# Kernel tuning notes

Measured on AMD Instinct MI355X. Metric: run time of the kernel, lower is better.

The kernel has to match this reference:

```python
import jax, jax.numpy as jnp
import numpy as np
import math

ITER = 5
ALPHA = 2.0
C = 128
B, H, W = 64, 40, 96


def _conv(x, w, pad_h, pad_w):
    # x: [B,C,H,W], w: [O,I,kh,kw]
    return jax.lax.conv_general_dilated(
        x, w, window_strides=(1, 1),
        padding=[(pad_h, pad_h), (pad_w, pad_w)],
        dimension_numbers=("NCHW", "OIHW", "NCHW"))


def setup_inputs() -> dict:
    key = jax.random.key(0)
    k = jax.random.split(key, 5)
    bound = math.sqrt(2.0 / (C * 9 * 5))
    x = jax.random.normal(k[0], (B, C, H, W), dtype=jnp.float32)
    wd = jax.random.uniform(k[1], (ITER, C, C, 1, 9), jnp.float32, -bound, bound)
    wu = jax.random.uniform(k[2], (ITER, C, C, 1, 9), jnp.float32, -bound, bound)
    wr = jax.random.uniform(k[3], (ITER, C, C, 9, 1), jnp.float32, -bound, bound)
    wl = jax.random.uniform(k[4], (ITER, C, C, 9, 1), jnp.float32, -bound, bound)
    return {"x": x, "wd": wd, "wu": wu, "wr": wr, "wl": wl}


def reference(x, wd, wu, wr, wl):
    h, w = x.shape[-2], x.shape[-1]
    y = x
    # downward: circular shift of rows by +offset == roll(-offset) along H
    for i in range(ITER):
        off = h // 2 ** (ITER - i)
        y = y + ALPHA * jax.nn.relu(_conv(jnp.roll(y, -off, axis=2), wd[i], 0, 4))
    # upward: rows shifted by -offset == roll(+offset)
    for i in range(ITER):
        off = h // 2 ** (ITER - i)
        y = y + ALPHA * jax.nn.relu(_conv(jnp.roll(y, off, axis=2), wu[i], 0, 4))
    # rightward: cols shifted by +offset == roll(-offset) along W
    for i in range(ITER):
        off = w // 2 ** (ITER - i)
        y = y + ALPHA * jax.nn.relu(_conv(jnp.roll(y, -off, axis=3), wr[i], 4, 0))
    # leftward: cols shifted by -offset == roll(+offset)
    for i in range(ITER):
        off = w // 2 ** (ITER - i)
        y = y + ALPHA * jax.nn.relu(_conv(jnp.roll(y, off, axis=3), wl[i], 4, 0))
    return y
```

## Files before the change

### kernel.cpp

```cpp
#include <hip/hip_runtime.h>
#include <cstdint>
#include <cstddef>

#define CH 128
#define HH 40
#define WW 96
#define BB 64
#define HW (HH*WW)
#define CHW ((size_t)CH*HW)

typedef _Float16 half8  __attribute__((ext_vector_type(8)));
typedef _Float16 half4v __attribute__((ext_vector_type(4)));
typedef float    float4v __attribute__((ext_vector_type(4)));

#define MFMA16(a,b,c) __builtin_amdgcn_mfma_f32_16x16x32_f16((a),(b),(c),0,0,0)

#define SPLIT_SCALE 2048.0f
#define INV_SPLIT   (1.0f/2048.0f)

#define NHWC_HALVES (BB*HH*WW*CH)
#define WSTEP_F     (CH*CH*9)
#define WFRAG_HALVES (20*9*4*8*64*8)

__device__ __forceinline__ void gload16(const _Float16* g, _Float16* l) {
    __builtin_amdgcn_global_load_lds(
        (const __attribute__((address_space(1))) void*)g,
        (__attribute__((address_space(3))) void*)l,
        16, 0, 0);
}


__global__ __launch_bounds__(256) void prep_weights(
    const float* __restrict__ wd, const float* __restrict__ wu,
    const float* __restrict__ wr, const float* __restrict__ wl,
    _Float16* __restrict__ WH, _Float16* __restrict__ WM)
{
    const int bx = blockIdx.x;
    const int s = bx / 9, t = bx % 9;
    const float* src;
    if (s < 5)       src = wd + (size_t)s*WSTEP_F;
    else if (s < 10) src = wu + (size_t)(s-5)*WSTEP_F;
    else if (s < 15) src = wr + (size_t)(s-10)*WSTEP_F;
    else             src = wl + (size_t)(s-15)*WSTEP_F;

    for (int idx = threadIdx.x; idx < 2048; idx += 256) {
        const int lane = idx & 63;
        const int mt   = (idx >> 6) & 7;
        const int kq   = idx >> 9;
        const int co   = mt*16 + (lane & 15);
        const int cib  = kq*32 + (lane >> 4)*8;
        const int F    = ((((s*9 + t)*4 + kq)*8 + mt)*64 + lane)*8;
        #pragma unroll
        for (int j = 0; j < 8; ++j) {
            const float w = src[(size_t)(co*CH + (cib + j))*9 + t];
            const _Float16 h = (_Float16)w;
            WH[F + j] = h;
            WM[F + j] = (_Float16)((w - (float)h) * SPLIT_SCALE);
        }
    }
}

__global__ __launch_bounds__(256) void prep_acts(
    const float* __restrict__ x, _Float16* __restrict__ H, _Float16* __restrict__ M)
{
    __shared__ float tile[CH][33];
    const int wt = blockIdx.x, h = blockIdx.y, b = blockIdx.z;
    const int tid = threadIdx.x;
    {
        const int wl = tid & 31, c0 = tid >> 5;
        for (int it = 0; it < 16; ++it) {
            const int ci = it*8 + c0;
            tile[ci][wl] = x[((size_t)(b*CH + ci)*HH + h)*WW + wt*32 + wl];
        }
    }
    __syncthreads();
    {
        const int ci = tid & 127, w0 = tid >> 7;
        for (int it = 0; it < 16; ++it) {
            const int wl = it*2 + w0;
            const float v = tile[ci][wl];
            const _Float16 hh = (_Float16)v;
            const int o = ((b*HH + h)*WW + wt*32 + wl)*CH + ci;
            H[o] = hh;
            M[o] = (_Float16)((v - (float)hh) * SPLIT_SCALE);
        }
    }
}

__global__ __launch_bounds__(256, 2) void hconv_mfma(
    const _Float16* __restrict__ srcH, const _Float16* __restrict__ srcM,
    _Float16* __restrict__ dstH, _Float16* __restrict__ dstM,
    const _Float16* __restrict__ WH, const _Float16* __restrict__ WM,
    int s, int hoff)
{
    __shared__ _Float16 sB[2][104*128];
    const int h = blockIdx.x, b = blockIdx.y;
    const int tid = threadIdx.x;
    const int hp = (h + hoff) % HH;
    const int lane = tid & 63, wave = tid >> 6;

    {
        const int rr = lane >> 4, slot = lane & 15;
        #pragma unroll
        for (int k = 0; k < 6; ++k) {
            const int c = wave*6 + k;
            const int rbase = 4 + 4*c;
            const int row = rbase + rr;
            const size_t goff = ((size_t)(b*HH + hp)*WW + (rbase - 4))*CH;
            const int so = rr*CH + ((slot ^ (row & 7))*8);
            gload16(srcH + goff + so, (_Float16*)&sB[0][rbase*128]);
            gload16(srcM + goff + so, (_Float16*)&sB[1][rbase*128]);
        }
        const int zrow = (wave & 1)*100;
        const int arr  = wave >> 1;
        *(half8*)&sB[arr][zrow*128 + lane*8] = (half8){};
    }
    __syncthreads();

    const int n = lane & 15, quad = lane >> 4;
    const int mgrp = wave & 1, ngrp = wave >> 1;
    const int qs = quad*8;
#define BADDR(row, kq) ((row)*128 + ((((kq)*32) + qs) ^ ((((row) & 7)) << 3)))

    float4v acc0[4][3], acc1[4][3];
    #pragma unroll
    for (int i = 0; i < 4; ++i)
        #pragma unroll
        for (int j = 0; j < 3; ++j) {
            acc0[i][j] = (float4v){0.f,0.f,0.f,0.f};
            acc1[i][j] = (float4v){0.f,0.f,0.f,0.f};
        }

    int rowb[3];
    #pragma unroll
    for (int j = 0; j < 3; ++j) rowb[j] = (ngrp*3 + j)*16 + n;

    const size_t Fb = (size_t)s*147456 + (size_t)(mgrp*2048 + lane*8);

    half8 Wh[2][4], Wm[2][4];
    #pragma unroll
    for (int i = 0; i < 4; ++i) {
        Wh[0][i] = *(const half8*)(WH + Fb + i*512);
        Wm[0][i] = *(const half8*)(WM + Fb + i*512);
    }
    half8 pbh = *(const half8*)&sB[0][BADDR(rowb[0], 0)];
    half8 pbm = *(const half8*)&sB[1][BADDR(rowb[0], 0)];

    for (int t = 0; t < 9; ++t) {
        #pragma unroll
        for (int kq = 0; kq < 4; ++kq) {
            const int it  = t*4 + kq;
            const int itn = (it < 35) ? it + 1 : 35;
            const int pc  = kq & 1;
            const int pn  = pc ^ 1;
            {
                const _Float16* nH = WH + Fb + (size_t)itn*4096;
                const _Float16* nM = WM + Fb + (size_t)itn*4096;
                #pragma unroll
                for (int i = 0; i < 4; ++i) {
                    Wh[pn][i] = *(const half8*)(nH + i*512);
                    Wm[pn][i] = *(const half8*)(nM + i*512);
                }
            }
            const int tn = itn >> 2, kqn = itn & 3;
            #pragma unroll
            for (int j = 0; j < 3; ++j) {
                const half8 bh = pbh, bm = pbm;
                int nro;
                if (j < 2) nro = BADDR(rowb[j+1] + t, kq);
                else       nro = BADDR(rowb[0] + tn, kqn);
                pbh = *(const half8*)&sB[0][nro];
                pbm = *(const half8*)&sB[1][nro];
                __builtin_amdgcn_s_setprio(1);
                #pragma unroll
                for (int i = 0; i < 4; ++i) {
                    acc0[i][j] = MFMA16(Wh[pc][i], bh, acc0[i][j]);
                    acc1[i][j] = MFMA16(Wh[pc][i], bm, acc1[i][j]);
                    acc1[i][j] = MFMA16(Wm[pc][i], bh, acc1[i][j]);
                }
                __builtin_amdgcn_s_setprio(0);
            }
        }
    }
#undef BADDR

    const int spbase = (b*HH + h)*WW;
    #pragma unroll
    for (int i = 0; i < 4; ++i) {
        const int co = (mgrp*4 + i)*16 + quad*4;
        #pragma unroll
        for (int j = 0; j < 3; ++j) {
            const int w  = (ngrp*3 + j)*16 + n;
            const int sp = (spbase + w)*CH + co;
            const half4v oh = *(const half4v*)(srcH + sp);
            const half4v om = *(const half4v*)(srcM + sp);
            half4v zh, zm;
            #pragma unroll
            for (int r = 0; r < 4; ++r) {
                const float v = acc0[i][j][r] + acc1[i][j][r]*INV_SPLIT;
                const float y = (float)oh[r] + (float)om[r]*INV_SPLIT;
                const float z = y + 2.0f*fmaxf(v, 0.0f);
                const _Float16 a = (_Float16)z;
                zh[r] = a;
                zm[r] = (_Float16)((z - (float)a)*SPLIT_SCALE);
            }
            *(half4v*)(dstH + sp) = zh;
            *(half4v*)(dstM + sp) = zm;
        }
    }
}

__global__ __launch_bounds__(256, 2) void vconv_mfma(
    const _Float16* __restrict__ srcH, const _Float16* __restrict__ srcM,
    _Float16* __restrict__ dstH, _Float16* __restrict__ dstM,
    const _Float16* __restrict__ WH, const _Float16* __restrict__ WM,
    int s, int woff, int final, float* __restrict__ f32out)
{
    __shared__ _Float16 sB[2][96*128];
    const int wp = blockIdx.x, b = blockIdx.y;
    const int tid = threadIdx.x;
    const int lane = tid & 63, wave = tid >> 6;

    {
        const int rr = lane >> 4, slot = lane & 15;
        for (int k = wave; k < 20; k += 4) {
            const int col = (k >= 10);
            const int c = k - col*10;
            const int rbase = col*48 + 4 + 4*c;
            const int h0 = 4*c;
            const int wsrc = (wp*2 + col + woff) % WW;
            const size_t goff = ((size_t)(b*HH + h0)*WW + wsrc)*CH;
            const int row = rbase + rr;
            const int so = rr*(WW*CH) + ((slot ^ (row & 7))*8);
            gload16(srcH + goff + so, (_Float16*)&sB[0][rbase*128]);
            gload16(srcM + goff + so, (_Float16*)&sB[1][rbase*128]);
        }
        const int zrow = (wave & 1)*44 + (wave >> 1)*48;
        *(half8*)&sB[0][zrow*128 + lane*8] = (half8){};
        *(half8*)&sB[1][zrow*128 + lane*8] = (half8){};
    }
    __syncthreads();

    const int n = lane & 15, quad = lane >> 4;
    const int mgrp = wave & 1;
    const int jbase = (wave >> 1)*3;
    const bool has3 = (wave >> 1) == 0;
    const int qs = quad*8;
#define BADDR(row, kq) ((row)*128 + ((((kq)*32) + qs) ^ ((((row) & 7)) << 3)))

    float4v acc0[4][3], acc1[4][3];
    #pragma unroll
    for (int i = 0; i < 4; ++i)
        #pragma unroll
        for (int j = 0; j < 3; ++j) {
            acc0[i][j] = (float4v){0.f,0.f,0.f,0.f};
            acc1[i][j] = (float4v){0.f,0.f,0.f,0.f};
        }

    int rowbse[3];
    #pragma unroll
    for (int jj = 0; jj < 3; ++jj) {
        int o = (jbase + jj)*16 + n;
        if (o > 79) o = 79;
        const int col = (o >= 40);
        rowbse[jj] = o + 8*col;
    }

    const size_t Fb = (size_t)s*147456 + (size_t)(mgrp*2048 + lane*8);

    half8 Wh[2][4], Wm[2][4];
    #pragma unroll
    for (int i = 0; i < 4; ++i) {
        Wh[0][i] = *(const half8*)(WH + Fb + i*512);
        Wm[0][i] = *(const half8*)(WM + Fb + i*512);
    }
    half8 pbh = *(const half8*)&sB[0][BADDR(rowbse[0], 0)];
    half8 pbm = *(const half8*)&sB[1][BADDR(rowbse[0], 0)];

    for (int t = 0; t < 9; ++t) {
        #pragma unroll
        for (int kq = 0; kq < 4; ++kq) {
            const int it  = t*4 + kq;
            const int itn = (it < 35) ? it + 1 : 35;
            const int pc  = kq & 1;
            const int pn  = pc ^ 1;
            {
                const _Float16* nH = WH + Fb + (size_t)itn*4096;
                const _Float16* nM = WM + Fb + (size_t)itn*4096;
                #pragma unroll
                for (int i = 0; i < 4; ++i) {
                    Wh[pn][i] = *(const half8*)(nH + i*512);
                    Wm[pn][i] = *(const half8*)(nM + i*512);
                }
            }
            const int tn = itn >> 2, kqn = itn & 3;
            #pragma unroll
            for (int jj = 0; jj < 3; ++jj) {
                if (jj != 2 || has3) {
                    const half8 bh = pbh, bm = pbm;
                    int nro;
                    if (jj == 0)      nro = BADDR(rowbse[1] + t, kq);
                    else if (jj == 1) nro = has3 ? BADDR(rowbse[2] + t, kq)
                                                 : BADDR(rowbse[0] + tn, kqn);
                    else              nro = BADDR(rowbse[0] + tn, kqn);
                    pbh = *(const half8*)&sB[0][nro];
                    pbm = *(const half8*)&sB[1][nro];
                    __builtin_amdgcn_s_setprio(1);
                    #pragma unroll
                    for (int i = 0; i < 4; ++i) {
                        acc0[i][jj] = MFMA16(Wh[pc][i], bh, acc0[i][jj]);
                        acc1[i][jj] = MFMA16(Wh[pc][i], bm, acc1[i][jj]);
                        acc1[i][jj] = MFMA16(Wm[pc][i], bh, acc1[i][jj]);
                    }
                    __builtin_amdgcn_s_setprio(0);
                }
            }
        }
    }
#undef BADDR

    #pragma unroll
    for (int i = 0; i < 4; ++i) {
        const int co = (mgrp*4 + i)*16 + quad*4;
        #pragma unroll
        for (int jj = 0; jj < 3; ++jj) {
            if (jj != 2 || has3) {
                const int o = (jbase + jj)*16 + n;
                const int col = (o >= 40);
                const int h_out = o - 40*col;
                const int w_out = wp*2 + col;
                const int sp = ((b*HH + h_out)*WW + w_out)*CH + co;
                const half4v oh = *(const half4v*)(srcH + sp);
                const half4v om = *(const half4v*)(srcM + sp);
                if (final) {
                    float4v z4;
                    #pragma unroll
                    for (int r = 0; r < 4; ++r) {
                        const float v = acc0[i][jj][r] + acc1[i][jj][r]*INV_SPLIT;
                        const float y = (float)oh[r] + (float)om[r]*INV_SPLIT;
                        z4[r] = y + 2.0f*fmaxf(v, 0.0f);
                    }
                    *(float4v*)(f32out + sp) = z4;
                } else {
                    half4v zh, zm;
                    #pragma unroll
                    for (int r = 0; r < 4; ++r) {
                        const float v = acc0[i][jj][r] + acc1[i][jj][r]*INV_SPLIT;
                        const float y = (float)oh[r] + (float)om[r]*INV_SPLIT;
                        const float z = y + 2.0f*fmaxf(v, 0.0f);
                        const _Float16 a = (_Float16)z;
                        zh[r] = a;
                        zm[r] = (_Float16)((z - (float)a)*SPLIT_SCALE);
                    }
                    *(half4v*)(dstH + sp) = zh;
                    *(half4v*)(dstM + sp) = zm;
                }
            }
        }
    }
}

__global__ __launch_bounds__(256) void nhwc_to_nchw(
    const float* __restrict__ src, float* __restrict__ dst)
{
    __shared__ float tile[32][133];
    const int wt = blockIdx.x, h = blockIdx.y, b = blockIdx.z;
    const int tid = threadIdx.x;
    {
        const int ci = tid & 127, w0 = tid >> 7;
        for (int it = 0; it < 16; ++it) {
            const int wl = it*2 + w0;
            tile[wl][ci] = src[((size_t)(b*HH + h)*WW + wt*32 + wl)*CH + ci];
        }
    }
    __syncthreads();
    {
        const int wl = tid & 31, c0 = tid >> 5;
        for (int it = 0; it < 16; ++it) {
            const int ci = it*8 + c0;
            dst[((size_t)(b*CH + ci)*HH + h)*WW + wt*32 + wl] = tile[wl][ci];
        }
    }
}

__global__ __launch_bounds__(256) void hconv_step(
    const float* __restrict__ src, const float* __restrict__ wgt,
    float* __restrict__ dst, int hoff)
{
    __shared__ float ld[CH][104];
    const int h = blockIdx.x, b = blockIdx.y, tid = threadIdx.x;
    const int hp = (h + hoff) % HH;
    const float* srow = src + (size_t)b*CHW + (size_t)hp*WW;
    for (int idx = tid; idx < CH*24; idx += 256) {
        int ci = idx / 24, j = idx % 24;
        float4 v = *reinterpret_cast<const float4*>(srow + (size_t)ci*HW + j*4);
        *reinterpret_cast<float4*>(&ld[ci][4 + 4*j]) = v;
    }
    if (tid < CH) {
        *reinterpret_cast<float4*>(&ld[tid][0])   = make_float4(0.f,0.f,0.f,0.f);
        *reinterpret_cast<float4*>(&ld[tid][100]) = make_float4(0.f,0.f,0.f,0.f);
    }
    __syncthreads();
    const int tx = tid & 7, ty = tid >> 3;
    const int w0 = tx*12, co0 = ty*4;
    float acc[4][12];
    #pragma unroll
    for (int c = 0; c < 4; ++c)
        #pragma unroll
        for (int k = 0; k < 12; ++k) acc[c][k] = 0.f;
    const float* wb = wgt + (size_t)co0*(CH*9);
    for (int ci = 0; ci < CH; ++ci) {
        float xr[20];
        #pragma unroll
        for (int j = 0; j < 5; ++j) {
            float4 v = *reinterpret_cast<const float4*>(&ld[ci][w0 + 4*j]);
            xr[4*j+0]=v.x; xr[4*j+1]=v.y; xr[4*j+2]=v.z; xr[4*j+3]=v.w;
        }
        #pragma unroll
        for (int c = 0; c < 4; ++c) {
            const float* wp = wb + (size_t)c*(CH*9) + ci*9;
            #pragma unroll
            for (int t = 0; t < 9; ++t) {
                const float wv = wp[t];
                #pragma unroll
                for (int k = 0; k < 12; ++k) acc[c][k] = fmaf(wv, xr[k+t], acc[c][k]);
            }
        }
    }
    const size_t obase = (size_t)b*CHW + (size_t)h*WW + w0;
    #pragma unroll
    for (int c = 0; c < 4; ++c) {
        const size_t o = obase + (size_t)(co0 + c)*HW;
        #pragma unroll
        for (int j = 0; j < 3; ++j) {
            float4 s = *reinterpret_cast<const float4*>(src + o + 4*j);
            float4 r;
            r.x = s.x + 2.f*fmaxf(acc[c][4*j+0], 0.f);
            r.y = s.y + 2.f*fmaxf(acc[c][4*j+1], 0.f);
            r.z = s.z + 2.f*fmaxf(acc[c][4*j+2], 0.f);
            r.w = s.w + 2.f*fmaxf(acc[c][4*j+3], 0.f);
            *reinterpret_cast<float4*>(dst + o + 4*j) = r;
        }
    }
}

__global__ __launch_bounds__(256) void vconv_step(
    const float* __restrict__ src, const float* __restrict__ wgt,
    float* __restrict__ dst, int woff)
{
    __shared__ float ld[CH][2][48];
    const int w0 = blockIdx.x*2, b = blockIdx.y, tid = threadIdx.x;
    const int w1 = (w0 + woff) % WW, w2 = (w0 + 1 + woff) % WW;
    const float* sb = src + (size_t)b*CHW;
    for (int idx = tid; idx < CH*HH; idx += 256) {
        int ci = idx / HH, hh = idx % HH;
        const float* p = sb + (size_t)ci*HW + (size_t)hh*WW;
        ld[ci][0][4 + hh] = p[w1];
        ld[ci][1][4 + hh] = p[w2];
    }
    if (tid < CH) {
        #pragma unroll
        for (int j = 0; j < 4; ++j) {
            ld[tid][0][j]=0.f; ld[tid][0][44+j]=0.f;
            ld[tid][1][j]=0.f; ld[tid][1][44+j]=0.f;
        }
    }
    __syncthreads();
    const int tx = tid & 7, ty = tid >> 3;
    const int wi = tx >> 2, h0 = (tx & 3)*10, co0 = ty*4;
    float acc[4][10];
    #pragma unroll
    for (int c = 0; c < 4; ++c)
        #pragma unroll
        for (int k = 0; k < 10; ++k) acc[c][k] = 0.f;
    const float* wb = wgt + (size_t)co0*(CH*9);
    for (int ci = 0; ci < CH; ++ci) {
        float xr[18];
        #pragma unroll
        for (int j = 0; j < 18; ++j) xr[j] = ld[ci][wi][h0 + j];
        #pragma unroll
        for (int c = 0; c < 4; ++c) {
            const float* wp = wb + (size_t)c*(CH*9) + ci*9;
            #pragma unroll
            for (int t = 0; t < 9; ++t) {
                const float wv = wp[t];
                #pragma unroll
                for (int k = 0; k < 10; ++k) acc[c][k] = fmaf(wv, xr[k+t], acc[c][k]);
            }
        }
    }
    #pragma unroll
    for (int c = 0; c < 4; ++c) {
        const size_t o = (size_t)b*CHW + (size_t)(co0 + c)*HW + (size_t)h0*WW + (w0 + wi);
        #pragma unroll
        for (int k = 0; k < 10; ++k) {
            const float s = src[o + (size_t)k*WW];
            dst[o + (size_t)k*WW] = s + 2.f*fmaxf(acc[c][k], 0.f);
        }
    }
}

extern "C" void kernel_launch(void* const* d_in, const int* in_sizes, int n_in,
                              void* d_out, int out_size, void* d_ws, size_t ws_size,
                              hipStream_t stream)
{
    const float* x  = (const float*)d_in[0];
    const float* wd = (const float*)d_in[1];
    const float* wu = (const float*)d_in[2];
    const float* wr = (const float*)d_in[3];
    const float* wl = (const float*)d_in[4];

    const size_t NEED = 125829120ULL + 2ULL*WFRAG_HALVES*2ULL;

    if (ws_size >= NEED) {
        _Float16* HA  = (_Float16*)d_ws;
        _Float16* MA  = HA + NHWC_HALVES;
        _Float16* WHp = (_Float16*)((char*)d_ws + 125829120ULL);
        _Float16* WMp = WHp + WFRAG_HALVES;
        _Float16* HB  = (_Float16*)d_out;
        _Float16* MB  = HB + NHWC_HALVES;
        float* f32tmp = (float*)d_ws;

        prep_weights<<<dim3(180), 256, 0, stream>>>(wd, wu, wr, wl, WHp, WMp);
        prep_acts<<<dim3(3, HH, BB), 256, 0, stream>>>(x, HA, MA);

        const int hoffs[10] = {1,2,5,10,20, 39,38,35,30,20};
        for (int s = 0; s < 10; ++s) {
            const _Float16* sH = (s & 1) ? HB : HA;
            const _Float16* sM = (s & 1) ? MB : MA;
            _Float16* dH = (s & 1) ? HA : HB;
            _Float16* dM = (s & 1) ? MA : MB;
            hconv_mfma<<<dim3(HH, BB), 256, 0, stream>>>(sH, sM, dH, dM,
                                                         WHp, WMp, s, hoffs[s]);
        }
        const int woffs[10] = {3,6,12,24,48, 93,90,84,72,48};
        for (int k = 0; k < 10; ++k) {
            const int s = 10 + k;
            const _Float16* sH = (s & 1) ? HB : HA;
            const _Float16* sM = (s & 1) ? MB : MA;
            _Float16* dH = (s & 1) ? HA : HB;
            _Float16* dM = (s & 1) ? MA : MB;
            const int fin = (s == 19);
            vconv_mfma<<<dim3(WW/2, BB), 256, 0, stream>>>(sH, sM, dH, dM,
                                                           WHp, WMp, s, woffs[k],
                                                           fin, f32tmp);
        }
        nhwc_to_nchw<<<dim3(3, HH, BB), 256, 0, stream>>>(f32tmp, (float*)d_out);
    } else {
        float* out = (float*)d_out;
        float* ws  = (float*)d_ws;
        const size_t WSTEP = (size_t)WSTEP_F;
        const int hoffs[5] = {1, 2, 5, 10, 20};
        const int woffs[5] = {3, 6, 12, 24, 48};
        dim3 hgrid(HH, BB), vgrid(WW/2, BB);
        const float* src = x;
        int step = 0;
        for (int i = 0; i < 5; ++i) {
            float* dst = (step & 1) ? out : ws;
            hconv_step<<<hgrid, 256, 0, stream>>>(src, wd + i*WSTEP, dst, hoffs[i]);
            src = dst; ++step;
        }
        for (int i = 0; i < 5; ++i) {
            float* dst = (step & 1) ? out : ws;
            hconv_step<<<hgrid, 256, 0, stream>>>(src, wu + i*WSTEP, dst, (HH - hoffs[i]) % HH);
            src = dst; ++step;
        }
        for (int i = 0; i < 5; ++i) {
            float* dst = (step & 1) ? out : ws;
            vconv_step<<<vgrid, 256, 0, stream>>>(src, wr + i*WSTEP, dst, woffs[i]);
            src = dst; ++step;
        }
        for (int i = 0; i < 5; ++i) {
            float* dst = (step & 1) ? out : ws;
            vconv_step<<<vgrid, 256, 0, stream>>>(src, wl + i*WSTEP, dst, (WW - woffs[i]) % WW);
            src = dst; ++step;
        }
    }
}
```

Before: 4.485 ms.

## Repartition vertical conv wave tiles to split output channels across four waves

Changes how the four waves split the 128x80 output tile of the column-direction conv kernel. Before, waves were split 2 ways over output channels (64 each) and 2 ways over spatial positions (3 and 2 N-tiles, uneven). Now each wave owns 32 output channels and all 5 spatial N-tiles. This removes the load imbalance where half the waves did 2/3 of the work. In exchange, each wave reads every B fragment from LDS, which raises LDS traffic, while per-wave weight register and global load volume is halved.

```diff
diff --git a/kernel.cpp b/kernel.cpp
--- a/kernel.cpp
+++ b/kernel.cpp
@@ -242,35 +242,31 @@
     __syncthreads();
 
     const int n = lane & 15, quad = lane >> 4;
-    const int mgrp = wave & 1;
-    const int jbase = (wave >> 1)*3;
-    const bool has3 = (wave >> 1) == 0;
     const int qs = quad*8;
 #define BADDR(row, kq) ((row)*128 + ((((kq)*32) + qs) ^ ((((row) & 7)) << 3)))
 
-    float4v acc0[4][3], acc1[4][3];
-    #pragma unroll
-    for (int i = 0; i < 4; ++i)
-        #pragma unroll
-        for (int j = 0; j < 3; ++j) {
+    float4v acc0[2][5], acc1[2][5];
+    #pragma unroll
+    for (int i = 0; i < 2; ++i)
+        #pragma unroll
+        for (int j = 0; j < 5; ++j) {
             acc0[i][j] = (float4v){0.f,0.f,0.f,0.f};
             acc1[i][j] = (float4v){0.f,0.f,0.f,0.f};
         }
 
-    int rowbse[3];
-    #pragma unroll
-    for (int jj = 0; jj < 3; ++jj) {
-        int o = (jbase + jj)*16 + n;
-        if (o > 79) o = 79;
+    int rowbse[5];
+    #pragma unroll
+    for (int j = 0; j < 5; ++j) {
+        const int o = j*16 + n;
         const int col = (o >= 40);
-        rowbse[jj] = o + 8*col;
-    }
-
-    const size_t Fb = (size_t)s*147456 + (size_t)(mgrp*2048 + lane*8);
-
-    half8 Wh[2][4], Wm[2][4];
-    #pragma unroll
-    for (int i = 0; i < 4; ++i) {
+        rowbse[j] = o + 8*col;
+    }
+
+    const size_t Fb = (size_t)s*147456 + (size_t)(wave*1024 + lane*8);
+
+    half8 Wh[2][2], Wm[2][2];
+    #pragma unroll
+    for (int i = 0; i < 2; ++i) {
         Wh[0][i] = *(const half8*)(WH + Fb + i*512);
         Wm[0][i] = *(const half8*)(WM + Fb + i*512);
     }
@@ -288,73 +284,68 @@
                 const _Float16* nH = WH + Fb + (size_t)itn*4096;
                 const _Float16* nM = WM + Fb + (size_t)itn*4096;
                 #pragma unroll
-                for (int i = 0; i < 4; ++i) {
+                for (int i = 0; i < 2; ++i) {
                     Wh[pn][i] = *(const half8*)(nH + i*512);
                     Wm[pn][i] = *(const half8*)(nM + i*512);
                 }
             }
             const int tn = itn >> 2, kqn = itn & 3;
             #pragma unroll
-            for (int jj = 0; jj < 3; ++jj) {
-                if (jj != 2 || has3) {
-                    const half8 bh = pbh, bm = pbm;
-                    int nro;
-                    if (jj == 0)      nro = BADDR(rowbse[1] + t, kq);
-                    else if (jj == 1) nro = has3 ? BADDR(rowbse[2] + t, kq)
-                                                 : BADDR(rowbse[0] + tn, kqn);
-                    else              nro = BADDR(rowbse[0] + tn, kqn);
-                    pbh = *(const half8*)&sB[0][nro];
-                    pbm = *(const half8*)&sB[1][nro];
-                    __builtin_amdgcn_s_setprio(1);
-                    #pragma unroll
-                    for (int i = 0; i < 4; ++i) {
-                        acc0[i][jj] = MFMA16(Wh[pc][i], bh, acc0[i][jj]);
-                        acc1[i][jj] = MFMA16(Wh[pc][i], bm, acc1[i][jj]);
-                        acc1[i][jj] = MFMA16(Wm[pc][i], bh, acc1[i][jj]);
-                    }
-                    __builtin_amdgcn_s_setprio(0);
+            for (int j = 0; j < 5; ++j) {
+                const half8 bh = pbh, bm = pbm;
+                const int nro = (j < 4) ? BADDR(rowbse[j+1] + t, kq)
+                                        : BADDR(rowbse[0] + tn, kqn);
+                pbh = *(const half8*)&sB[0][nro];
+                pbm = *(const half8*)&sB[1][nro];
+                __builtin_amdgcn_s_setprio(1);
+                #pragma unroll
+                for (int i = 0; i < 2; ++i) {
+                    acc0[i][j] = MFMA16(Wh[pc][i], bh, acc0[i][j]);
+                    acc1[i][j] = MFMA16(Wh[pc][i], bm, acc1[i][j]);
                 }
+                #pragma unroll
+                for (int i = 0; i < 2; ++i)
+                    acc1[i][j] = MFMA16(Wm[pc][i], bh, acc1[i][j]);
+                __builtin_amdgcn_s_setprio(0);
             }
         }
     }
 #undef BADDR
 
     #pragma unroll
-    for (int i = 0; i < 4; ++i) {
-        const int co = (mgrp*4 + i)*16 + quad*4;
-        #pragma unroll
-        for (int jj = 0; jj < 3; ++jj) {
-            if (jj != 2 || has3) {
-                const int o = (jbase + jj)*16 + n;
-                const int col = (o >= 40);
-                const int h_out = o - 40*col;
-                const int w_out = wp*2 + col;
-                const int sp = ((b*HH + h_out)*WW + w_out)*CH + co;
-                const half4v oh = *(const half4v*)(srcH + sp);
-                const half4v om = *(const half4v*)(srcM + sp);
-                if (final) {
-                    float4v z4;
-                    #pragma unroll
-                    for (int r = 0; r < 4; ++r) {
-                        const float v = acc0[i][jj][r] + acc1[i][jj][r]*INV_SPLIT;
-                        const float y = (float)oh[r] + (float)om[r]*INV_SPLIT;
-                        z4[r] = y + 2.0f*fmaxf(v, 0.0f);
-                    }
-                    *(float4v*)(f32out + sp) = z4;
-                } else {
-                    half4v zh, zm;
-                    #pragma unroll
-                    for (int r = 0; r < 4; ++r) {
-                        const float v = acc0[i][jj][r] + acc1[i][jj][r]*INV_SPLIT;
-                        const float y = (float)oh[r] + (float)om[r]*INV_SPLIT;
-                        const float z = y + 2.0f*fmaxf(v, 0.0f);
-                        const _Float16 a = (_Float16)z;
-                        zh[r] = a;
-                        zm[r] = (_Float16)((z - (float)a)*SPLIT_SCALE);
-                    }
-                    *(half4v*)(dstH + sp) = zh;
-                    *(half4v*)(dstM + sp) = zm;
+    for (int i = 0; i < 2; ++i) {
+        const int co = (wave*2 + i)*16 + quad*4;
+        #pragma unroll
+        for (int j = 0; j < 5; ++j) {
+            const int o = j*16 + n;
+            const int col = (o >= 40);
+            const int h_out = o - 40*col;
+            const int w_out = wp*2 + col;
+            const int sp = ((b*HH + h_out)*WW + w_out)*CH + co;
+            const half4v oh = *(const half4v*)(srcH + sp);
+            const half4v om = *(const half4v*)(srcM + sp);
+            if (final) {
+                float4v z4;
+                #pragma unroll
+                for (int r = 0; r < 4; ++r) {
+                    const float v = acc0[i][j][r] + acc1[i][j][r]*INV_SPLIT;
+                    const float y = (float)oh[r] + (float)om[r]*INV_SPLIT;
+                    z4[r] = y + 2.0f*fmaxf(v, 0.0f);
                 }
+                *(float4v*)(f32out + sp) = z4;
+            } else {
+                half4v zh, zm;
+                #pragma unroll
+                for (int r = 0; r < 4; ++r) {
+                    const float v = acc0[i][j][r] + acc1[i][j][r]*INV_SPLIT;
+                    const float y = (float)oh[r] + (float)om[r]*INV_SPLIT;
+                    const float z = y + 2.0f*fmaxf(v, 0.0f);
+                    const _Float16 a = (_Float16)z;
+                    zh[r] = a;
+                    zm[r] = (_Float16)((z - (float)a)*SPLIT_SCALE);
+                }
+                *(half4v*)(dstH + sp) = zh;
+                *(half4v*)(dstM + sp) = zm;
             }
         }
     }
```

Measured after the change: 4.080 ms. 1.1x faster.
